# Kernel optimization log

Measured on AMD Instinct MI355X. Metric: run time of the kernel, lower is better.

Reference implementation:

```python
import jax, jax.numpy as jnp
import numpy as np

N_DET = 32

def _nuc_features(nuc_coords, nuc_charges, nuc_mask):
    # masked mean-centering of nuclear coords, then concat charge feature
    m = nuc_mask[:, None].astype(nuc_coords.dtype)  # [n_nuc, 1]
    mean = (nuc_coords * m).sum(0, keepdims=True) / jnp.maximum(m.sum(0, keepdims=True), 1.0)
    centered = nuc_coords - mean
    feats = jnp.concatenate([nuc_charges[:, None], centered], axis=-1)  # [n_nuc, 4]
    return feats * m

def _spin_orbitals(e_coords, e_mask, nuc_coords, feats, nuc_mask, W_pi, W_zeta):
    # exponent factors / nuclear weights via per-nucleus linear maps, then transpose
    zeta = (feats @ W_pi).T   # exponent_factors [n_det*max_e, n_nuc]
    pi = (feats @ W_zeta).T   # nuclear_weights  [n_det*max_e, n_nuc]
    # masked pairwise electron-nucleus distances
    diff = e_coords[:, None, :] - nuc_coords[None, :, :]          # [n_e, n_nuc, 3]
    dist_mask = e_mask[:, None] & nuc_mask[None, :]               # [n_e, n_nuc]
    d2 = (diff * diff).sum(-1)
    dist = jnp.sqrt(jnp.where(dist_mask, d2, 1.0))                # safe sqrt on masked entries
    # exp-decay envelope, masked, weighted sum over nuclei
    expo = jnp.where(dist_mask[:, None, :],
                     jnp.exp(-jnp.abs(dist[:, None, :] * zeta[None])), 0.0)  # [n_e, nd*me, n_nuc]
    orb = (pi[None] * expo).sum(-1)                               # [n_e, nd*me]
    n_e = e_coords.shape[0]
    orb = orb.reshape(n_e, N_DET, -1).swapaxes(-2, -3)            # [n_det, n_e, max_e]
    sm = e_mask[:, None] & e_mask[None, :]
    return jnp.where(sm, orb, jnp.eye(n_e, dtype=orb.dtype))


def setup_inputs() -> dict:
    key = jax.random.key(0)
    ks = jax.random.split(key, 8)
    ME, MN = 128, 128
    f = jnp.float32
    return {
        "up_coords": jax.random.normal(ks[0], (ME, 3), f),
        "down_coords": jax.random.normal(ks[1], (ME, 3), f),
        "nuc_coords": jax.random.normal(ks[2], (MN, 3), f),
        "nuc_charges": jax.random.uniform(ks[3], (MN,), f),
        "W_pi_up": jax.random.normal(ks[4], (4, N_DET * ME), f),
        "W_zeta_up": jax.random.normal(ks[5], (4, N_DET * ME), f),
        "W_pi_down": jax.random.normal(ks[6], (4, N_DET * ME), f),
        "W_zeta_down": jax.random.normal(ks[7], (4, N_DET * ME), f),
        "up_mask": jnp.ones((ME,), bool),
        "down_mask": jnp.ones((ME,), bool),
        "nuc_mask": jnp.ones((MN,), bool),
    }


def reference(up_coords, down_coords, nuc_coords, nuc_charges,
              W_pi_up, W_zeta_up, W_pi_down, W_zeta_down,
              up_mask, down_mask, nuc_mask):
    feats = _nuc_features(nuc_coords, nuc_charges, nuc_mask)
    up = _spin_orbitals(up_coords, up_mask, nuc_coords, feats, nuc_mask, W_pi_up, W_zeta_up)
    down = _spin_orbitals(down_coords, down_mask, nuc_coords, feats, nuc_mask, W_pi_down, W_zeta_down)
    return jnp.stack([up, down])  # [2, n_det, n_e, max_e]
```

## Files before the change

kernel.cpp:

```cpp
#include <hip/hip_runtime.h>
#include <cstddef>

#define NDET 32
#define ME   128
#define MN   128
#define NOUT (NDET * ME)
#define LOG2E 1.4426950408889634f

#if __has_builtin(__builtin_amdgcn_exp2f)
#define EXP2(x) __builtin_amdgcn_exp2f(x)
#else
#define EXP2(x) exp2f(x)
#endif

typedef float v2f __attribute__((ext_vector_type(2)));

__global__ __launch_bounds__(512) void env_kernel(
    const float* __restrict__ up_coords,
    const float* __restrict__ down_coords,
    const float* __restrict__ nuc_coords,
    const float* __restrict__ nuc_charges,
    const float* __restrict__ W_pi_up,
    const float* __restrict__ W_zeta_up,
    const float* __restrict__ W_pi_down,
    const float* __restrict__ W_zeta_down,
    float* __restrict__ out)
{
    __shared__ float4 feats4[MN];
    __shared__ float  duv[MN * 16];
    __shared__ float  ecl[16 * 3];
    __shared__ float  msum[2][3];

    const int tid = (int)threadIdx.x;
    const int e0  = (int)blockIdx.x * 16;
    const int d   = (int)blockIdx.y;
    const int s   = (int)blockIdx.z;

    const float* ec = s ? down_coords : up_coords;
    const float* We = s ? W_pi_down   : W_pi_up;
    const float* Ww = s ? W_zeta_down : W_zeta_up;

    if (tid < MN) {
        feats4[tid] = make_float4(nuc_charges[tid],
                                  nuc_coords[tid * 3 + 0],
                                  nuc_coords[tid * 3 + 1],
                                  nuc_coords[tid * 3 + 2]);
    } else if (tid < MN + 48) {
        ecl[tid - MN] = ec[e0 * 3 + (tid - MN)];
    }
    __syncthreads();

    if (tid < MN) {
        float4 f = feats4[tid];
        float sx = f.y, sy = f.z, sz = f.w;
        #pragma unroll
        for (int off = 32; off > 0; off >>= 1) {
            sx += __shfl_xor(sx, off);
            sy += __shfl_xor(sy, off);
            sz += __shfl_xor(sz, off);
        }
        if ((tid & 63) == 0) {
            const int w = tid >> 6;
            msum[w][0] = sx; msum[w][1] = sy; msum[w][2] = sz;
        }
    }
    __syncthreads();

    const float mx = (msum[0][0] + msum[1][0]) * (1.f / MN);
    const float my = (msum[0][1] + msum[1][1]) * (1.f / MN);
    const float mz = (msum[0][2] + msum[1][2]) * (1.f / MN);

    {
        const int n = tid >> 2;
        const int q = tid & 3;
        const float4 f = feats4[n];
        float r[4];
        #pragma unroll
        for (int i = 0; i < 4; ++i) {
            const int e = q * 4 + i;
            const float dx = ecl[e * 3 + 0] - f.y;
            const float dy = ecl[e * 3 + 1] - f.z;
            const float dz = ecl[e * 3 + 2] - f.w;
            r[i] = sqrtf(fmaf(dx, dx, fmaf(dy, dy, dz * dz))) * (-LOG2E);
        }
        *(float4*)&duv[n * 16 + q * 4] = make_float4(r[0], r[1], r[2], r[3]);
    }
    __syncthreads();

    if (tid < MN) {
        float4 f = feats4[tid];
        feats4[tid] = make_float4(f.x, f.y - mx, f.z - my, f.w - mz);
    }
    __syncthreads();

    const int j  = tid & 127;
    const int g  = tid >> 7;
    const int h  = g & 1;
    const int nh = g >> 1;
    const int o  = d * ME + j;

    const v2f w0 = { We[0*NOUT+o], Ww[0*NOUT+o] };
    const v2f w1 = { We[1*NOUT+o], Ww[1*NOUT+o] };
    const v2f w2 = { We[2*NOUT+o], Ww[2*NOUT+o] };
    const v2f w3 = { We[3*NOUT+o], Ww[3*NOUT+o] };

    v2f acc01 = {0.f, 0.f}, acc23 = {0.f, 0.f}, acc45 = {0.f, 0.f}, acc67 = {0.f, 0.f};

    const float4* du4 = (const float4*)duv;
    const int nbeg = nh * 64;
    #pragma unroll 8
    for (int n = nbeg; n < nbeg + 64; ++n) {
        const float4 f = feats4[n];
        v2f zp = f.x * w0 + (f.y * w1 + (f.z * w2 + f.w * w3));
        const float az = __builtin_fabsf(zp.x);
        const v2f az2 = {az, az};
        const v2f pi2 = {zp.y, zp.y};
        const float4 u0 = du4[n * 4 + h * 2 + 0];
        const float4 u1 = du4[n * 4 + h * 2 + 1];
        v2f t01 = (v2f){u0.x, u0.y} * az2;
        v2f t23 = (v2f){u0.z, u0.w} * az2;
        v2f t45 = (v2f){u1.x, u1.y} * az2;
        v2f t67 = (v2f){u1.z, u1.w} * az2;
        t01.x = EXP2(t01.x); t01.y = EXP2(t01.y);
        t23.x = EXP2(t23.x); t23.y = EXP2(t23.y);
        t45.x = EXP2(t45.x); t45.y = EXP2(t45.y);
        t67.x = EXP2(t67.x); t67.y = EXP2(t67.y);
        acc01 = acc01 + pi2 * t01;
        acc23 = acc23 + pi2 * t23;
        acc45 = acc45 + pi2 * t45;
        acc67 = acc67 + pi2 * t67;
    }

    __syncthreads();
    if (nh) {
        float4* r = (float4*)&duv[(h * 128 + j) * 8];
        r[0] = make_float4(acc01.x, acc01.y, acc23.x, acc23.y);
        r[1] = make_float4(acc45.x, acc45.y, acc67.x, acc67.y);
    }
    __syncthreads();
    if (!nh) {
        const float4* r = (const float4*)&duv[(h * 128 + j) * 8];
        const float4 p0 = r[0];
        const float4 p1 = r[1];
        const int e_base = e0 + h * 8;
        float* op = out + ((((size_t)s * NDET + d) * ME + e_base) * ME + j);
        op[0 * ME] = acc01.x + p0.x;
        op[1 * ME] = acc01.y + p0.y;
        op[2 * ME] = acc23.x + p0.z;
        op[3 * ME] = acc23.y + p0.w;
        op[4 * ME] = acc45.x + p1.x;
        op[5 * ME] = acc45.y + p1.y;
        op[6 * ME] = acc67.x + p1.z;
        op[7 * ME] = acc67.y + p1.w;
    }
}

extern "C" void kernel_launch(void* const* d_in, const int* in_sizes, int n_in,
                              void* d_out, int out_size, void* d_ws, size_t ws_size,
                              hipStream_t stream)
{
    (void)in_sizes; (void)n_in; (void)out_size; (void)d_ws; (void)ws_size;
    env_kernel<<<dim3(8, 32, 2), 512, 0, stream>>>(
        (const float*)d_in[0],
        (const float*)d_in[1],
        (const float*)d_in[2],
        (const float*)d_in[3],
        (const float*)d_in[4],
        (const float*)d_in[5],
        (const float*)d_in[6],
        (const float*)d_in[7],
        (float*)d_out);
}
```

Before: 90.18 us.

## Halve electrons per block and split nuclei four ways across wave groups

Each block now handles 8 electrons instead of 16, which doubles the grid to 1024 blocks. The 512 threads are split into four groups of 32 nuclei each instead of two halves of electrons times two halves of nuclei. Partial sums go through a dedicated shared buffer and are reduced by group 0, and a min-blocks hint of 8 is added to launch bounds. The aim is more parallelism and occupancy on the MI355X's many CUs. The cost is that the per-block setup (feature mean, zeta/pi matmul per nucleus) is redone twice as often, and the reduction adds work.

```diff
diff --git a/kernel.cpp b/kernel.cpp
--- a/kernel.cpp
+++ b/kernel.cpp
@@ -4,6 +4,7 @@
 #define NDET 32
 #define ME   128
 #define MN   128
+#define EBLK 8
 #define NOUT (NDET * ME)
 #define LOG2E 1.4426950408889634f
 
@@ -15,7 +16,7 @@
 
 typedef float v2f __attribute__((ext_vector_type(2)));
 
-__global__ __launch_bounds__(512) void env_kernel(
+__global__ __launch_bounds__(512, 8) void env_kernel(
     const float* __restrict__ up_coords,
     const float* __restrict__ down_coords,
     const float* __restrict__ nuc_coords,
@@ -27,12 +28,13 @@
     float* __restrict__ out)
 {
     __shared__ float4 feats4[MN];
-    __shared__ float  duv[MN * 16];
-    __shared__ float  ecl[16 * 3];
+    __shared__ float  duv[MN * EBLK];
+    __shared__ float  ecl[EBLK * 3];
     __shared__ float  msum[2][3];
+    __shared__ float4 red[3][128][2];
 
     const int tid = (int)threadIdx.x;
-    const int e0  = (int)blockIdx.x * 16;
+    const int e0  = (int)blockIdx.x * EBLK;
     const int d   = (int)blockIdx.y;
     const int s   = (int)blockIdx.z;
 
@@ -45,7 +47,7 @@
                                   nuc_coords[tid * 3 + 0],
                                   nuc_coords[tid * 3 + 1],
                                   nuc_coords[tid * 3 + 2]);
-    } else if (tid < MN + 48) {
+    } else if (tid < MN + EBLK * 3) {
         ecl[tid - MN] = ec[e0 * 3 + (tid - MN)];
     }
     __syncthreads();
@@ -74,16 +76,16 @@
         const int n = tid >> 2;
         const int q = tid & 3;
         const float4 f = feats4[n];
-        float r[4];
+        float r[2];
         #pragma unroll
-        for (int i = 0; i < 4; ++i) {
-            const int e = q * 4 + i;
+        for (int i = 0; i < 2; ++i) {
+            const int e = q * 2 + i;
             const float dx = ecl[e * 3 + 0] - f.y;
             const float dy = ecl[e * 3 + 1] - f.z;
             const float dz = ecl[e * 3 + 2] - f.w;
             r[i] = sqrtf(fmaf(dx, dx, fmaf(dy, dy, dz * dz))) * (-LOG2E);
         }
-        *(float4*)&duv[n * 16 + q * 4] = make_float4(r[0], r[1], r[2], r[3]);
+        *(float2*)&duv[n * EBLK + q * 2] = make_float2(r[0], r[1]);
     }
     __syncthreads();
 
@@ -93,11 +95,9 @@
     }
     __syncthreads();
 
-    const int j  = tid & 127;
-    const int g  = tid >> 7;
-    const int h  = g & 1;
-    const int nh = g >> 1;
-    const int o  = d * ME + j;
+    const int j = tid & 127;
+    const int g = tid >> 7;
+    const int o = d * ME + j;
 
     const v2f w0 = { We[0*NOUT+o], Ww[0*NOUT+o] };
     const v2f w1 = { We[1*NOUT+o], Ww[1*NOUT+o] };
@@ -107,16 +107,16 @@
     v2f acc01 = {0.f, 0.f}, acc23 = {0.f, 0.f}, acc45 = {0.f, 0.f}, acc67 = {0.f, 0.f};
 
     const float4* du4 = (const float4*)duv;
-    const int nbeg = nh * 64;
+    const int nbeg = g * 32;
     #pragma unroll 8
-    for (int n = nbeg; n < nbeg + 64; ++n) {
+    for (int n = nbeg; n < nbeg + 32; ++n) {
         const float4 f = feats4[n];
         v2f zp = f.x * w0 + (f.y * w1 + (f.z * w2 + f.w * w3));
         const float az = __builtin_fabsf(zp.x);
         const v2f az2 = {az, az};
         const v2f pi2 = {zp.y, zp.y};
-        const float4 u0 = du4[n * 4 + h * 2 + 0];
-        const float4 u1 = du4[n * 4 + h * 2 + 1];
+        const float4 u0 = du4[n * 2 + 0];
+        const float4 u1 = du4[n * 2 + 1];
         v2f t01 = (v2f){u0.x, u0.y} * az2;
         v2f t23 = (v2f){u0.z, u0.w} * az2;
         v2f t45 = (v2f){u1.x, u1.y} * az2;
@@ -131,19 +131,20 @@
         acc67 = acc67 + pi2 * t67;
     }
 
-    __syncthreads();
-    if (nh) {
-        float4* r = (float4*)&duv[(h * 128 + j) * 8];
-        r[0] = make_float4(acc01.x, acc01.y, acc23.x, acc23.y);
-        r[1] = make_float4(acc45.x, acc45.y, acc67.x, acc67.y);
+    if (g) {
+        red[g - 1][j][0] = make_float4(acc01.x, acc01.y, acc23.x, acc23.y);
+        red[g - 1][j][1] = make_float4(acc45.x, acc45.y, acc67.x, acc67.y);
     }
     __syncthreads();
-    if (!nh) {
-        const float4* r = (const float4*)&duv[(h * 128 + j) * 8];
-        const float4 p0 = r[0];
-        const float4 p1 = r[1];
-        const int e_base = e0 + h * 8;
-        float* op = out + ((((size_t)s * NDET + d) * ME + e_base) * ME + j);
+    if (!g) {
+        float4 p0 = red[0][j][0], p1 = red[0][j][1];
+        const float4 q0 = red[1][j][0], q1 = red[1][j][1];
+        const float4 r0 = red[2][j][0], r1 = red[2][j][1];
+        p0.x += q0.x + r0.x; p0.y += q0.y + r0.y;
+        p0.z += q0.z + r0.z; p0.w += q0.w + r0.w;
+        p1.x += q1.x + r1.x; p1.y += q1.y + r1.y;
+        p1.z += q1.z + r1.z; p1.w += q1.w + r1.w;
+        float* op = out + ((((size_t)s * NDET + d) * ME + e0) * ME + j);
         op[0 * ME] = acc01.x + p0.x;
         op[1 * ME] = acc01.y + p0.y;
         op[2 * ME] = acc23.x + p0.z;
@@ -160,7 +161,7 @@
                               hipStream_t stream)
 {
     (void)in_sizes; (void)n_in; (void)out_size; (void)d_ws; (void)ws_size;
-    env_kernel<<<dim3(8, 32, 2), 512, 0, stream>>>(
+    env_kernel<<<dim3(ME / EBLK, NDET, 2), 512, 0, stream>>>(
         (const float*)d_in[0],
         (const float*)d_in[1],
         (const float*)d_in[2],
```

Measured after the change: 89.78 us. Within noise of the previous version (-0.4%).
